# Kernel tuning notes

Hardware: AMD Instinct MI355X
Metric: run time of the kernel (lower is better)

## Reference

```python
import jax, jax.numpy as jnp
import numpy as np

DIM = 1024
HEADS = 8
DIM_HEAD = 64
INNER = HEADS * DIM_HEAD
SCALE = DIM_HEAD ** -0.5


def setup_inputs() -> dict:
    key = jax.random.key(0)
    ks = jax.random.split(key, 6)
    b, n = 2, 2048
    x = jax.random.normal(ks[0], (b, n, DIM), dtype=jnp.float32)
    rel_pos_bias = jax.random.normal(ks[1], (HEADS, n, n), dtype=jnp.float32)
    # learned params (Linear stores W as [out, in]; we keep [in, out] for x @ W)
    Wq = jax.random.normal(ks[2], (DIM, INNER), dtype=jnp.float32) * (DIM ** -0.5)
    Wkv = jax.random.normal(ks[3], (DIM, 2 * DIM_HEAD), dtype=jnp.float32) * (DIM ** -0.5)
    Wo = jax.random.normal(ks[4], (INNER, DIM), dtype=jnp.float32) * (INNER ** -0.5)
    bo = jax.random.normal(ks[5], (DIM,), dtype=jnp.float32) * 0.01
    return {"x": x, "rel_pos_bias": rel_pos_bias, "Wq": Wq, "Wkv": Wkv, "Wo": Wo, "bo": bo}


def reference(x, rel_pos_bias, Wq, Wkv, Wo, bo):
    b, n, _ = x.shape
    q = x @ Wq                       # [b, n, h*d]
    kv = x @ Wkv                     # [b, n, 2d] (multi-query: single shared kv head)
    k, v = kv[..., :DIM_HEAD], kv[..., DIM_HEAD:]
    q = q.reshape(b, n, HEADS, DIM_HEAD).transpose(0, 2, 1, 3) * SCALE  # [b, h, n, d]
    sim = jnp.einsum('bhid,bjd->bhij', q, k)
    sim = sim + rel_pos_bias         # bias broadcast over batch
    causal_mask = jnp.triu(jnp.ones((n, n), dtype=bool), k=1)
    neg = -jnp.finfo(sim.dtype).max
    sim = jnp.where(causal_mask, neg, sim)
    attn = jax.nn.softmax(sim, axis=-1)  # stable softmax (max-subtract internally)
    out = jnp.einsum('bhij,bjd->bhid', attn, v)
    out = out.transpose(0, 2, 1, 3).reshape(b, n, INNER)  # [b, n, h*d]
    return out @ Wo + bo
```

## Files before the change

kernel.cpp:

```cpp
#include <hip/hip_runtime.h>

#define NSEQ 2048
#define NB 2
#define NH 8
#define HD 64
#define DMODEL 1024
#define DINNER 512

#define SLOT_F 4224

typedef __attribute__((ext_vector_type(8))) short bf16x8;
typedef __attribute__((ext_vector_type(4))) float f32x4;

__device__ __forceinline__ ushort f2bf(float f) {
  uint u = __float_as_uint(f);
  uint r = (u + 0x7fffu + ((u >> 16) & 1u)) >> 16;
  return (ushort)r;
}

__device__ __forceinline__ void gld16(const ushort* g, ushort* l) {
  __builtin_amdgcn_global_load_lds(
      (const __attribute__((address_space(1))) uint*)g,
      (__attribute__((address_space(3))) uint*)l, 16, 0, 0);
}

__global__ __launch_bounds__(256) void cast_x_kernel(
    const float* __restrict__ x, ushort* __restrict__ xb) {
  size_t i = ((size_t)blockIdx.x * 256 + threadIdx.x) * 8;
  float4 a = *(const float4*)(x + i);
  float4 b = *(const float4*)(x + i + 4);
  ushort4 o1, o2;
  o1.x = f2bf(a.x); o1.y = f2bf(a.y); o1.z = f2bf(a.z); o1.w = f2bf(a.w);
  o2.x = f2bf(b.x); o2.y = f2bf(b.y); o2.z = f2bf(b.z); o2.w = f2bf(b.w);
  *(ushort4*)(xb + i) = o1;
  *(ushort4*)(xb + i + 4) = o2;
}

__global__ __launch_bounds__(256) void transpose_cast_kernel(
    const float* __restrict__ srcA, const float* __restrict__ srcB,
    int ldA, int ldB, int nsplit, int Ktot, ushort* __restrict__ dst) {
  __shared__ float t[64][65];
  const int k0 = blockIdx.x * 64;
  const int n0 = blockIdx.y * 64;
  const float* src; int ld, nb;
  if (n0 < nsplit) { src = srcA; ld = ldA; nb = n0; }
  else { src = srcB; ld = ldB; nb = n0 - nsplit; }
  const int r = threadIdx.x >> 4;
  const int c = (threadIdx.x & 15) * 4;
#pragma unroll
  for (int rr = r; rr < 64; rr += 16) {
    float4 v = *(const float4*)(src + (size_t)(k0 + rr) * ld + nb + c);
    t[rr][c + 0] = v.x; t[rr][c + 1] = v.y; t[rr][c + 2] = v.z; t[rr][c + 3] = v.w;
  }
  __syncthreads();
#pragma unroll
  for (int rr = r; rr < 64; rr += 16) {
    ushort4 o;
    o.x = f2bf(t[c + 0][rr]); o.y = f2bf(t[c + 1][rr]);
    o.z = f2bf(t[c + 2][rr]); o.w = f2bf(t[c + 3][rr]);
    *(ushort4*)(dst + (size_t)(n0 + rr) * Ktot + k0 + c) = o;
  }
}

__device__ __forceinline__ void stage_tile(const ushort* __restrict__ src, int ld,
                                           int row0, int k0, ushort* lds, int tid) {
#pragma unroll
  for (int i = 0; i < 4; ++i) {
    const int cix = i * 256 + tid;
    const int row = cix >> 3, j = cix & 7;
    uint4 v = *(const uint4*)(src + (size_t)(row0 + row) * ld + k0 + j * 8);
    *(uint4*)((char*)lds + row * 128 + ((j ^ (row & 7)) << 4)) = v;
  }
}

__device__ __forceinline__ void gemm_tile(const ushort* __restrict__ A,
                                          const ushort* __restrict__ Bt, int K,
                                          int m0, int n0, ushort* As, ushort* Bs,
                                          int tid, f32x4 acc[4][4]) {
  const int lane = tid & 63;
  const int w = tid >> 6;
  const int wr = w >> 1, wc = w & 1;
  const int lr = lane & 15, lg = lane >> 4;
  for (int k0 = 0; k0 < K; k0 += 64) {
    __syncthreads();
    stage_tile(A, K, m0, k0, As, tid);
    stage_tile(Bt, K, n0, k0, Bs, tid);
    __syncthreads();
#pragma unroll
    for (int kk = 0; kk < 2; ++kk) {
      bf16x8 af[4], bfr[4];
#pragma unroll
      for (int mi = 0; mi < 4; ++mi) {
        const int r = wr * 64 + mi * 16 + lr;
        af[mi] = *(const bf16x8*)((char*)As + r * 128 + (((kk * 4 + lg) ^ (r & 7)) << 4));
      }
#pragma unroll
      for (int ni = 0; ni < 4; ++ni) {
        const int r = wc * 64 + ni * 16 + lr;
        bfr[ni] = *(const bf16x8*)((char*)Bs + r * 128 + (((kk * 4 + lg) ^ (r & 7)) << 4));
      }
#pragma unroll
      for (int mi = 0; mi < 4; ++mi)
#pragma unroll
        for (int ni = 0; ni < 4; ++ni)
          acc[mi][ni] = __builtin_amdgcn_mfma_f32_16x16x32_bf16(af[mi], bfr[ni],
                                                                acc[mi][ni], 0, 0, 0);
    }
  }
}

__global__ __launch_bounds__(256) void qkv_mfma_kernel(
    const ushort* __restrict__ xb, const ushort* __restrict__ WT1,
    ushort* __restrict__ qb, ushort* __restrict__ ksw, ushort* __restrict__ vsw) {
  __shared__ ushort As[128 * 64];
  __shared__ ushort Bs[128 * 64];
  const int tid = threadIdx.x;
  const int m0 = blockIdx.x * 128, n0 = blockIdx.y * 128;
  f32x4 acc[4][4];
#pragma unroll
  for (int a = 0; a < 4; ++a)
#pragma unroll
    for (int b = 0; b < 4; ++b) acc[a][b] = (f32x4){0.f, 0.f, 0.f, 0.f};
  gemm_tile(xb, WT1, DMODEL, m0, n0, As, Bs, tid, acc);
  const int lane = tid & 63;
  const int w = tid >> 6;
  const int wr = w >> 1, wc = w & 1;
  const int lr = lane & 15, lg = lane >> 4;
#pragma unroll
  for (int mi = 0; mi < 4; ++mi)
#pragma unroll
    for (int ni = 0; ni < 4; ++ni) {
      const int n = n0 + wc * 64 + ni * 16 + lr;
      if (n >= 640) continue;
#pragma unroll
      for (int r = 0; r < 4; ++r) {
        const int m = m0 + wr * 64 + mi * 16 + lg * 4 + r;
        const int bb = m >> 11, key = m & (NSEQ - 1);
        const float v = acc[mi][ni][r];
        if (n < DINNER) {
          const int h = n >> 6, d = n & 63;
          qb[((size_t)((bb * NH + h) * NSEQ) + key) * HD + d] = f2bf(v * 0.125f);
        } else if (n < DINNER + HD) {
          const int d = n - DINNER;
          const int t = key >> 6, row = key & 63;
          const int ch = d >> 3, pos = d & 7;
          ksw[(size_t)((bb * 32 + t) * 64 + row) * 64 +
              ((ch ^ (row & 7)) << 3) + pos] = f2bf(v);
        } else {
          const int d = n - DINNER - HD;
          const int pr = key >> 7, kk = key & 127;
          const int ch = kk >> 3, pos = kk & 7;
          vsw[(size_t)((bb * 16 + pr) * 64 + d) * 128 +
              ((ch ^ (d & 15)) << 3) + pos] = f2bf(v);
        }
      }
    }
}

__global__ __launch_bounds__(256) void out_mfma_kernel(
    const ushort* __restrict__ ab, const ushort* __restrict__ WoT,
    const float* __restrict__ bo, float* __restrict__ out) {
  __shared__ ushort As[128 * 64];
  __shared__ ushort Bs[128 * 64];
  const int tid = threadIdx.x;
  const int m0 = blockIdx.x * 128, n0 = blockIdx.y * 128;
  f32x4 acc[4][4];
#pragma unroll
  for (int a = 0; a < 4; ++a)
#pragma unroll
    for (int b = 0; b < 4; ++b) acc[a][b] = (f32x4){0.f, 0.f, 0.f, 0.f};
  gemm_tile(ab, WoT, DINNER, m0, n0, As, Bs, tid, acc);
  const int lane = tid & 63;
  const int w = tid >> 6;
  const int wr = w >> 1, wc = w & 1;
  const int lr = lane & 15, lg = lane >> 4;
#pragma unroll
  for (int mi = 0; mi < 4; ++mi)
#pragma unroll
    for (int ni = 0; ni < 4; ++ni) {
      const int n = n0 + wc * 64 + ni * 16 + lr;
      const float bias = bo[n];
#pragma unroll
      for (int r = 0; r < 4; ++r) {
        const int m = m0 + wr * 64 + mi * 16 + lg * 4 + r;
        out[(size_t)m * DMODEL + n] = acc[mi][ni][r] + bias;
      }
    }
}

__global__ __launch_bounds__(256) void attn_mfma_kernel(
    const ushort* __restrict__ qb, const ushort* __restrict__ ksw,
    const ushort* __restrict__ vsw, const float* __restrict__ rpb,
    ushort* __restrict__ ob, float* __restrict__ scratch) {
  __shared__ ushort Ks[2 * 128 * 64];
  __shared__ ushort Vs[2 * 64 * 128];
  __shared__ ushort Ps[4 * 16 * 128];
  const int tid = threadIdx.x;
  const int lane = tid & 63;
  const int w = tid >> 6;
  const int id = blockIdx.x;
  const int bh = id & 15;
  int qt, ch, p0, p1, partial;
  if (id < 256) {
    qt = 16 + (id >> 4); ch = 0; p0 = 0; p1 = 8; partial = 1;
  } else if (id < 512) {
    qt = 31 - ((id - 256) >> 4); ch = 1; p0 = 8; p1 = (qt >> 1) + 1; partial = 1;
  } else {
    qt = 15 - ((id - 512) >> 4); ch = 0; p0 = 0; p1 = (qt >> 1) + 1; partial = 0;
  }
  const int bb = bh >> 3, h = bh & 7;
  const int q0 = qt * 64;
  const int lr = lane & 15;
  const int lg = lane >> 4;
  const int pdiag = qt >> 1;

  const ushort* kpair = ksw + (size_t)bb * 32 * 64 * 64;
  const ushort* vpair = vsw + (size_t)bb * 16 * 64 * 128;
  const ushort* ksrcw = kpair + w * 2048 + lane * 8;
  const ushort* vsrcw = vpair + w * 2048 + lane * 8;
  ushort* kdstw = Ks + w * 2048;
  ushort* vdstw = Vs + w * 2048;

#define ISSUE(pp, bsel)                                                     \
  {                                                                         \
    const ushort* _ks = ksrcw + (size_t)(pp) * 8192;                        \
    const ushort* _vs = vsrcw + (size_t)(pp) * 8192;                        \
    ushort* _kd = kdstw + (bsel) * 8192;                                    \
    ushort* _vd = vdstw + (bsel) * 8192;                                    \
    gld16(_ks + 0 * 512, _kd + 0 * 512);                                    \
    gld16(_ks + 1 * 512, _kd + 1 * 512);                                    \
    gld16(_ks + 2 * 512, _kd + 2 * 512);                                    \
    gld16(_ks + 3 * 512, _kd + 3 * 512);                                    \
    gld16(_vs + 0 * 512, _vd + 0 * 512);                                    \
    gld16(_vs + 1 * 512, _vd + 1 * 512);                                    \
    gld16(_vs + 2 * 512, _vd + 2 * 512);                                    \
    gld16(_vs + 3 * 512, _vd + 3 * 512);                                    \
  }

#define LOAD_BIAS(pp, dst)                                                  \
  {                                                                         \
    const float* _br = rpb + (size_t)h * NSEQ * NSEQ +                      \
                       (size_t)(q0 + w * 16 + lg * 4) * NSEQ +              \
                       (pp) * 128 + lr;                                     \
    _Pragma("unroll")                                                       \
    for (int _ct = 0; _ct < 8; ++_ct)                                       \
      _Pragma("unroll")                                                     \
      for (int _r = 0; _r < 4; ++_r)                                        \
        dst[_ct][_r] = _br[(size_t)_r * NSEQ + _ct * 16];                   \
  }

  bf16x8 qf[2];
  {
    const ushort* qrow =
        qb + ((size_t)(bh * NSEQ) + q0 + w * 16 + lr) * HD + lg * 8;
    qf[0] = *(const bf16x8*)qrow;
    qf[1] = *(const bf16x8*)(qrow + 32);
  }
  f32x4 oacc[4];
  float m_run[4], l_run[4];
#pragma unroll
  for (int r = 0; r < 4; ++r) { m_run[r] = -1e30f; l_run[r] = 0.f; }
#pragma unroll
  for (int dt = 0; dt < 4; ++dt) oacc[dt] = (f32x4){0.f, 0.f, 0.f, 0.f};

  float bias_c[8][4], bias_n[8][4];

  ISSUE(p0, 0);
  LOAD_BIAS(p0, bias_c);
  ISSUE(p0 + 1, 1);
  int curb = 0;

  for (int p = p0; p < p1; ++p) {
    if (p < p1 - 1) {
      asm volatile("s_waitcnt vmcnt(40)" ::: "memory");
    } else {
      asm volatile("s_waitcnt vmcnt(32)" ::: "memory");
    }
    __builtin_amdgcn_sched_barrier(0);
    __builtin_amdgcn_s_barrier();

    const char* Kc = (const char*)(Ks + curb * 8192);
    const char* Vc = (const char*)(Vs + curb * 8192);
    f32x4 s[8];
    __builtin_amdgcn_s_setprio(1);
#pragma unroll
    for (int ct = 0; ct < 8; ++ct) {
      s[ct] = (f32x4){0.f, 0.f, 0.f, 0.f};
      const int krow = ct * 16 + lr;
#pragma unroll
      for (int kk = 0; kk < 2; ++kk) {
        bf16x8 kf = *(const bf16x8*)(Kc + krow * 128 +
                                     (((kk * 4 + lg) ^ (krow & 7)) << 4));
        s[ct] = __builtin_amdgcn_mfma_f32_16x16x32_bf16(qf[kk], kf, s[ct], 0, 0, 0);
      }
    }
    __builtin_amdgcn_s_setprio(0);
    if (p + 1 < p1) LOAD_BIAS(p + 1, bias_n);
#pragma unroll
    for (int ct = 0; ct < 8; ++ct)
#pragma unroll
      for (int r = 0; r < 4; ++r) s[ct][r] += bias_c[ct][r];
    if (p == pdiag) {
      const int qrel = q0 + w * 16 + lg * 4;
#pragma unroll
      for (int ct = 0; ct < 8; ++ct) {
        const int kg = p * 128 + ct * 16 + lr;
#pragma unroll
        for (int r = 0; r < 4; ++r)
          if (kg > qrel + r) s[ct][r] = -1e30f;
      }
    }
    float fac[4];
#pragma unroll
    for (int r = 0; r < 4; ++r) {
      float mt = s[0][r];
#pragma unroll
      for (int ct = 1; ct < 8; ++ct) mt = fmaxf(mt, s[ct][r]);
#pragma unroll
      for (int msk = 1; msk < 16; msk <<= 1)
        mt = fmaxf(mt, __shfl_xor(mt, msk, 64));
      const float m_new = fmaxf(m_run[r], mt);
      fac[r] = __expf(m_run[r] - m_new);
      m_run[r] = m_new;
      float ls = 0.f;
#pragma unroll
      for (int ct = 0; ct < 8; ++ct) {
        const float pv = __expf(s[ct][r] - m_new);
        s[ct][r] = pv;
        ls += pv;
      }
#pragma unroll
      for (int msk = 1; msk < 16; msk <<= 1) ls += __shfl_xor(ls, msk, 64);
      l_run[r] = l_run[r] * fac[r] + ls;
    }
#pragma unroll
    for (int dt = 0; dt < 4; ++dt)
#pragma unroll
      for (int r = 0; r < 4; ++r) oacc[dt][r] *= fac[r];
    char* Pw = (char*)Ps + w * 4096;
#pragma unroll
    for (int ct = 0; ct < 8; ++ct) {
      uint u01, u23;
      asm("v_cvt_pk_bf16_f32 %0, %1, %2" : "=v"(u01) : "v"(s[ct][0]), "v"(s[ct][1]));
      asm("v_cvt_pk_bf16_f32 %0, %1, %2" : "=v"(u23) : "v"(s[ct][2]), "v"(s[ct][3]));
      const int cbyte = (ct * 16 + lr) * 2;
      const int chv = cbyte >> 4, off = cbyte & 15;
      const int r0 = lg * 4;
      *(ushort*)(Pw + (r0 + 0) * 256 + (((chv ^ (r0 + 0)) << 4) | off)) = (ushort)u01;
      *(ushort*)(Pw + (r0 + 1) * 256 + (((chv ^ (r0 + 1)) << 4) | off)) = (ushort)(u01 >> 16);
      *(ushort*)(Pw + (r0 + 2) * 256 + (((chv ^ (r0 + 2)) << 4) | off)) = (ushort)u23;
      *(ushort*)(Pw + (r0 + 3) * 256 + (((chv ^ (r0 + 3)) << 4) | off)) = (ushort)(u23 >> 16);
    }
    __builtin_amdgcn_s_setprio(1);
#pragma unroll
    for (int kk = 0; kk < 4; ++kk) {
      bf16x8 pf = *(const bf16x8*)(Pw + lr * 256 + (((kk * 4 + lg) ^ lr) << 4));
#pragma unroll
      for (int dt = 0; dt < 4; ++dt) {
        const int vrow = dt * 16 + lr;
        bf16x8 vf = *(const bf16x8*)(Vc + vrow * 256 +
                                     (((kk * 4 + lg) ^ (vrow & 15)) << 4));
        oacc[dt] =
            __builtin_amdgcn_mfma_f32_16x16x32_bf16(pf, vf, oacc[dt], 0, 0, 0);
      }
    }
    __builtin_amdgcn_s_setprio(0);
    __builtin_amdgcn_sched_barrier(0);
    __builtin_amdgcn_s_barrier();
    if (p + 2 < p1) ISSUE(p + 2, curb);
    if (p + 1 < p1) {
#pragma unroll
      for (int ct = 0; ct < 8; ++ct)
#pragma unroll
        for (int r = 0; r < 4; ++r) bias_c[ct][r] = bias_n[ct][r];
    }
    curb ^= 1;
  }
#undef ISSUE
#undef LOAD_BIAS
  if (!partial) {
#pragma unroll
    for (int r = 0; r < 4; ++r) {
      const int qg = q0 + w * 16 + lg * 4 + r;
      const float inv = 1.0f / l_run[r];
      ushort* dst = ob + ((size_t)(bb * NSEQ) + qg) * DINNER + h * HD + lr;
#pragma unroll
      for (int dt = 0; dt < 4; ++dt) dst[dt * 16] = f2bf(oacc[dt][r] * inv);
    }
  } else {
    float* slot =
        scratch + (size_t)((bh * 16 + (qt - 16)) * 2 + ch) * SLOT_F;
#pragma unroll
    for (int r = 0; r < 4; ++r) {
      const int row = w * 16 + lg * 4 + r;
#pragma unroll
      for (int dt = 0; dt < 4; ++dt)
        slot[row * 64 + dt * 16 + lr] = oacc[dt][r];
      if (lr == 0) {
        slot[4096 + row] = m_run[r];
        slot[4160 + row] = l_run[r];
      }
    }
  }
}

__global__ __launch_bounds__(256) void attn_merge_kernel(
    const float* __restrict__ scratch, ushort* __restrict__ ob) {
  const int bid = blockIdx.x;
  const int bh = bid >> 4;
  const int qt = 16 + (bid & 15);
  const int bb = bh >> 3, h = bh & 7;
  const float* s0 = scratch + (size_t)((bh * 16 + (qt - 16)) * 2) * SLOT_F;
  const float* s1 = s0 + SLOT_F;
  const int t = threadIdx.x;
  const int r = t >> 2;
  const int c0 = (t & 3) * 16;
  const float m0 = s0[4096 + r], m1 = s1[4096 + r];
  const float M = fmaxf(m0, m1);
  const float sc0 = __expf(m0 - M), sc1 = __expf(m1 - M);
  const float L = s0[4160 + r] * sc0 + s1[4160 + r] * sc1;
  const float inv = 1.0f / L;
  ushort* dst = ob + ((size_t)(bb * NSEQ) + qt * 64 + r) * DINNER + h * HD + c0;
#pragma unroll
  for (int j4 = 0; j4 < 4; ++j4) {
    float4 a = *(const float4*)(s0 + r * 64 + c0 + j4 * 4);
    float4 b = *(const float4*)(s1 + r * 64 + c0 + j4 * 4);
    dst[j4 * 4 + 0] = f2bf((a.x * sc0 + b.x * sc1) * inv);
    dst[j4 * 4 + 1] = f2bf((a.y * sc0 + b.y * sc1) * inv);
    dst[j4 * 4 + 2] = f2bf((a.z * sc0 + b.z * sc1) * inv);
    dst[j4 * 4 + 3] = f2bf((a.w * sc0 + b.w * sc1) * inv);
  }
}

extern "C" void kernel_launch(void* const* d_in, const int* in_sizes, int n_in,
                              void* d_out, int out_size, void* d_ws, size_t ws_size,
                              hipStream_t stream) {
  (void)in_sizes; (void)n_in; (void)out_size; (void)ws_size;
  const float* x = (const float*)d_in[0];
  const float* rpb = (const float*)d_in[1];
  const float* Wq = (const float*)d_in[2];
  const float* Wkv = (const float*)d_in[3];
  const float* Wo = (const float*)d_in[4];
  const float* bo = (const float*)d_in[5];
  float* out = (float*)d_out;

  ushort* qbb = (ushort*)d_ws;
  ushort* ksw = qbb + (size_t)NB * NH * NSEQ * HD;
  ushort* vsw = ksw + (size_t)NB * NSEQ * HD;
  ushort* obuf = vsw + (size_t)NB * NSEQ * HD;
  ushort* xb = obuf + (size_t)NB * NSEQ * DINNER;
  ushort* WT1 = xb + (size_t)NB * NSEQ * DMODEL;
  ushort* WoT = WT1 + (size_t)640 * DMODEL;
  float* scratch = (float*)(WoT + (size_t)DMODEL * DINNER);

  cast_x_kernel<<<dim3(2048), 256, 0, stream>>>(x, xb);
  transpose_cast_kernel<<<dim3(16, 10), 256, 0, stream>>>(Wq, Wkv, 512, 128, 512,
                                                          DMODEL, WT1);
  transpose_cast_kernel<<<dim3(8, 16), 256, 0, stream>>>(Wo, Wo, DMODEL, DMODEL,
                                                         DMODEL, DINNER, WoT);
  qkv_mfma_kernel<<<dim3(32, 5), 256, 0, stream>>>(xb, WT1, qbb, ksw, vsw);
  attn_mfma_kernel<<<dim3(768), 256, 0, stream>>>(qbb, ksw, vsw, rpb, obuf,
                                                  scratch);
  attn_merge_kernel<<<dim3(256), 256, 0, stream>>>(scratch, obuf);
  out_mfma_kernel<<<dim3(32, 8), 256, 0, stream>>>(obuf, WoT, bo, out);
}
```

Measured before the change: 95.66 us.

## Transpose attention MFMA accumulators so each lane owns a query row, use exp2

Swaps the MFMA operand order so the score and output accumulators are transposed, which gives each lane a single query row and four consecutive keys. Row max and sum then need only two cross-lane shuffles instead of four per row, the bias loads become vectorized f32x4 reads, and P stores and output writes are packed. The softmax scale is folded into log2e so exp2 replaces expf, and the vmcnt thresholds are lowered to match the smaller number of bias loads. A wrong vmcnt count or a mismatch in the transposed layout would break correctness.

```diff
diff --git a/kernel.cpp b/kernel.cpp
--- a/kernel.cpp
+++ b/kernel.cpp
@@ -8,6 +8,7 @@
 #define DINNER 512
 
 #define SLOT_F 4224
+#define LOG2E 1.44269504f
 
 typedef __attribute__((ext_vector_type(8))) short bf16x8;
 typedef __attribute__((ext_vector_type(4))) float f32x4;
@@ -139,7 +140,8 @@
         const float v = acc[mi][ni][r];
         if (n < DINNER) {
           const int h = n >> 6, d = n & 63;
-          qb[((size_t)((bb * NH + h) * NSEQ) + key) * HD + d] = f2bf(v * 0.125f);
+          qb[((size_t)((bb * NH + h) * NSEQ) + key) * HD + d] =
+              f2bf(v * (0.125f * LOG2E));
         } else if (n < DINNER + HD) {
           const int d = n - DINNER;
           const int t = key >> 6, row = key & 63;
@@ -200,7 +202,7 @@
   const int w = tid >> 6;
   const int id = blockIdx.x;
   const int bh = id & 15;
-  int qt, ch, p0, p1, partial;
+  int qt, p0, p1, partial, ch;
   if (id < 256) {
     qt = 16 + (id >> 4); ch = 0; p0 = 0; p1 = 8; partial = 1;
   } else if (id < 512) {
@@ -213,6 +215,7 @@
   const int lr = lane & 15;
   const int lg = lane >> 4;
   const int pdiag = qt >> 1;
+  const int qg = q0 + w * 16 + lr;
 
   const ushort* kpair = ksw + (size_t)bb * 32 * 64 * 64;
   const ushort* vpair = vsw + (size_t)bb * 16 * 64 * 128;
@@ -240,30 +243,24 @@
 #define LOAD_BIAS(pp, dst)                                                  \
   {                                                                         \
     const float* _br = rpb + (size_t)h * NSEQ * NSEQ +                      \
-                       (size_t)(q0 + w * 16 + lg * 4) * NSEQ +              \
-                       (pp) * 128 + lr;                                     \
+                       (size_t)qg * NSEQ + (pp) * 128 + lg * 4;             \
     _Pragma("unroll")                                                       \
     for (int _ct = 0; _ct < 8; ++_ct)                                       \
-      _Pragma("unroll")                                                     \
-      for (int _r = 0; _r < 4; ++_r)                                        \
-        dst[_ct][_r] = _br[(size_t)_r * NSEQ + _ct * 16];                   \
+      dst[_ct] = *(const f32x4*)(_br + _ct * 16);                           \
   }
 
   bf16x8 qf[2];
   {
-    const ushort* qrow =
-        qb + ((size_t)(bh * NSEQ) + q0 + w * 16 + lr) * HD + lg * 8;
+    const ushort* qrow = qb + ((size_t)(bh * NSEQ) + qg) * HD + lg * 8;
     qf[0] = *(const bf16x8*)qrow;
     qf[1] = *(const bf16x8*)(qrow + 32);
   }
-  f32x4 oacc[4];
-  float m_run[4], l_run[4];
-#pragma unroll
-  for (int r = 0; r < 4; ++r) { m_run[r] = -1e30f; l_run[r] = 0.f; }
-#pragma unroll
-  for (int dt = 0; dt < 4; ++dt) oacc[dt] = (f32x4){0.f, 0.f, 0.f, 0.f};
-
-  float bias_c[8][4], bias_n[8][4];
+  f32x4 oaccT[4];
+#pragma unroll
+  for (int dt = 0; dt < 4; ++dt) oaccT[dt] = (f32x4){0.f, 0.f, 0.f, 0.f};
+  float m_run = -1e30f, l_run = 0.f;
+
+  f32x4 bias_c[8], bias_n[8];
 
   ISSUE(p0, 0);
   LOAD_BIAS(p0, bias_c);
@@ -272,9 +269,9 @@
 
   for (int p = p0; p < p1; ++p) {
     if (p < p1 - 1) {
-      asm volatile("s_waitcnt vmcnt(40)" ::: "memory");
+      asm volatile("s_waitcnt vmcnt(16)" ::: "memory");
     } else {
-      asm volatile("s_waitcnt vmcnt(32)" ::: "memory");
+      asm volatile("s_waitcnt vmcnt(8)" ::: "memory");
     }
     __builtin_amdgcn_sched_barrier(0);
     __builtin_amdgcn_s_barrier();
@@ -291,7 +288,7 @@
       for (int kk = 0; kk < 2; ++kk) {
         bf16x8 kf = *(const bf16x8*)(Kc + krow * 128 +
                                      (((kk * 4 + lg) ^ (krow & 7)) << 4));
-        s[ct] = __builtin_amdgcn_mfma_f32_16x16x32_bf16(qf[kk], kf, s[ct], 0, 0, 0);
+        s[ct] = __builtin_amdgcn_mfma_f32_16x16x32_bf16(kf, qf[kk], s[ct], 0, 0, 0);
       }
     }
     __builtin_amdgcn_s_setprio(0);
@@ -299,57 +296,51 @@
 #pragma unroll
     for (int ct = 0; ct < 8; ++ct)
 #pragma unroll
-      for (int r = 0; r < 4; ++r) s[ct][r] += bias_c[ct][r];
+      for (int r = 0; r < 4; ++r)
+        s[ct][r] = fmaf(bias_c[ct][r], LOG2E, s[ct][r]);
     if (p == pdiag) {
-      const int qrel = q0 + w * 16 + lg * 4;
 #pragma unroll
       for (int ct = 0; ct < 8; ++ct) {
-        const int kg = p * 128 + ct * 16 + lr;
+        const int kg = p * 128 + ct * 16 + lg * 4;
 #pragma unroll
         for (int r = 0; r < 4; ++r)
-          if (kg > qrel + r) s[ct][r] = -1e30f;
-      }
-    }
-    float fac[4];
-#pragma unroll
-    for (int r = 0; r < 4; ++r) {
-      float mt = s[0][r];
-#pragma unroll
-      for (int ct = 1; ct < 8; ++ct) mt = fmaxf(mt, s[ct][r]);
-#pragma unroll
-      for (int msk = 1; msk < 16; msk <<= 1)
-        mt = fmaxf(mt, __shfl_xor(mt, msk, 64));
-      const float m_new = fmaxf(m_run[r], mt);
-      fac[r] = __expf(m_run[r] - m_new);
-      m_run[r] = m_new;
-      float ls = 0.f;
-#pragma unroll
-      for (int ct = 0; ct < 8; ++ct) {
-        const float pv = __expf(s[ct][r] - m_new);
-        s[ct][r] = pv;
-        ls += pv;
-      }
-#pragma unroll
-      for (int msk = 1; msk < 16; msk <<= 1) ls += __shfl_xor(ls, msk, 64);
-      l_run[r] = l_run[r] * fac[r] + ls;
-    }
-#pragma unroll
-    for (int dt = 0; dt < 4; ++dt)
-#pragma unroll
-      for (int r = 0; r < 4; ++r) oacc[dt][r] *= fac[r];
+          if (kg + r > qg) s[ct][r] = -1e30f;
+      }
+    }
+    float cm[8];
+#pragma unroll
+    for (int ct = 0; ct < 8; ++ct)
+      cm[ct] = fmaxf(fmaxf(s[ct][0], s[ct][1]), fmaxf(s[ct][2], s[ct][3]));
+    float mt = fmaxf(fmaxf(fmaxf(cm[0], cm[1]), fmaxf(cm[2], cm[3])),
+                     fmaxf(fmaxf(cm[4], cm[5]), fmaxf(cm[6], cm[7])));
+    mt = fmaxf(mt, __shfl_xor(mt, 16, 64));
+    mt = fmaxf(mt, __shfl_xor(mt, 32, 64));
+    const float m_new = fmaxf(m_run, mt);
+    const float fac = exp2f(m_run - m_new);
+    m_run = m_new;
+    float cs[8];
+#pragma unroll
+    for (int ct = 0; ct < 8; ++ct) {
+#pragma unroll
+      for (int r = 0; r < 4; ++r) s[ct][r] = exp2f(s[ct][r] - m_new);
+      cs[ct] = (s[ct][0] + s[ct][1]) + (s[ct][2] + s[ct][3]);
+    }
+    float ls = ((cs[0] + cs[1]) + (cs[2] + cs[3])) +
+               ((cs[4] + cs[5]) + (cs[6] + cs[7]));
+    ls += __shfl_xor(ls, 16, 64);
+    ls += __shfl_xor(ls, 32, 64);
+    l_run = l_run * fac + ls;
+#pragma unroll
+    for (int dt = 0; dt < 4; ++dt) oaccT[dt] *= fac;
     char* Pw = (char*)Ps + w * 4096;
 #pragma unroll
     for (int ct = 0; ct < 8; ++ct) {
       uint u01, u23;
       asm("v_cvt_pk_bf16_f32 %0, %1, %2" : "=v"(u01) : "v"(s[ct][0]), "v"(s[ct][1]));
       asm("v_cvt_pk_bf16_f32 %0, %1, %2" : "=v"(u23) : "v"(s[ct][2]), "v"(s[ct][3]));
-      const int cbyte = (ct * 16 + lr) * 2;
-      const int chv = cbyte >> 4, off = cbyte & 15;
-      const int r0 = lg * 4;
-      *(ushort*)(Pw + (r0 + 0) * 256 + (((chv ^ (r0 + 0)) << 4) | off)) = (ushort)u01;
-      *(ushort*)(Pw + (r0 + 1) * 256 + (((chv ^ (r0 + 1)) << 4) | off)) = (ushort)(u01 >> 16);
-      *(ushort*)(Pw + (r0 + 2) * 256 + (((chv ^ (r0 + 2)) << 4) | off)) = (ushort)u23;
-      *(ushort*)(Pw + (r0 + 3) * 256 + (((chv ^ (r0 + 3)) << 4) | off)) = (ushort)(u23 >> 16);
+      const int chunk = 2 * ct + (lg >> 1);
+      uint2 uv; uv.x = u01; uv.y = u23;
+      *(uint2*)(Pw + lr * 256 + (((chunk ^ lr) << 4) | ((lg & 1) * 8))) = uv;
     }
     __builtin_amdgcn_s_setprio(1);
 #pragma unroll
@@ -360,8 +351,8 @@
         const int vrow = dt * 16 + lr;
         bf16x8 vf = *(const bf16x8*)(Vc + vrow * 256 +
                                      (((kk * 4 + lg) ^ (vrow & 15)) << 4));
-        oacc[dt] =
-            __builtin_amdgcn_mfma_f32_16x16x32_bf16(pf, vf, oacc[dt], 0, 0, 0);
+        oaccT[dt] =
+            __builtin_amdgcn_mfma_f32_16x16x32_bf16(vf, pf, oaccT[dt], 0, 0, 0);
       }
     }
     __builtin_amdgcn_s_setprio(0);
@@ -370,36 +361,34 @@
     if (p + 2 < p1) ISSUE(p + 2, curb);
     if (p + 1 < p1) {
 #pragma unroll
-      for (int ct = 0; ct < 8; ++ct)
-#pragma unroll
-        for (int r = 0; r < 4; ++r) bias_c[ct][r] = bias_n[ct][r];
+      for (int ct = 0; ct < 8; ++ct) bias_c[ct] = bias_n[ct];
     }
     curb ^= 1;
   }
 #undef ISSUE
 #undef LOAD_BIAS
   if (!partial) {
-#pragma unroll
-    for (int r = 0; r < 4; ++r) {
-      const int qg = q0 + w * 16 + lg * 4 + r;
-      const float inv = 1.0f / l_run[r];
-      ushort* dst = ob + ((size_t)(bb * NSEQ) + qg) * DINNER + h * HD + lr;
-#pragma unroll
-      for (int dt = 0; dt < 4; ++dt) dst[dt * 16] = f2bf(oacc[dt][r] * inv);
+    const float inv = 1.0f / l_run;
+    ushort* dst = ob + ((size_t)(bb * NSEQ) + qg) * DINNER + h * HD;
+#pragma unroll
+    for (int dt = 0; dt < 4; ++dt) {
+      uint u01, u23;
+      const float o0 = oaccT[dt][0] * inv, o1 = oaccT[dt][1] * inv;
+      const float o2 = oaccT[dt][2] * inv, o3 = oaccT[dt][3] * inv;
+      asm("v_cvt_pk_bf16_f32 %0, %1, %2" : "=v"(u01) : "v"(o0), "v"(o1));
+      asm("v_cvt_pk_bf16_f32 %0, %1, %2" : "=v"(u23) : "v"(o2), "v"(o3));
+      uint2 uv; uv.x = u01; uv.y = u23;
+      *(uint2*)(dst + dt * 16 + lg * 4) = uv;
     }
   } else {
-    float* slot =
-        scratch + (size_t)((bh * 16 + (qt - 16)) * 2 + ch) * SLOT_F;
-#pragma unroll
-    for (int r = 0; r < 4; ++r) {
-      const int row = w * 16 + lg * 4 + r;
-#pragma unroll
-      for (int dt = 0; dt < 4; ++dt)
-        slot[row * 64 + dt * 16 + lr] = oacc[dt][r];
-      if (lr == 0) {
-        slot[4096 + row] = m_run[r];
-        slot[4160 + row] = l_run[r];
-      }
+    float* slot = scratch + (size_t)((bh * 16 + (qt - 16)) * 2 + ch) * SLOT_F;
+    const int row = w * 16 + lr;
+#pragma unroll
+    for (int dt = 0; dt < 4; ++dt)
+      *(f32x4*)(slot + row * 64 + dt * 16 + lg * 4) = oaccT[dt];
+    if (lg == 0) {
+      slot[4096 + row] = m_run;
+      slot[4160 + row] = l_run;
     }
   }
 }
@@ -417,7 +406,7 @@
   const int c0 = (t & 3) * 16;
   const float m0 = s0[4096 + r], m1 = s1[4096 + r];
   const float M = fmaxf(m0, m1);
-  const float sc0 = __expf(m0 - M), sc1 = __expf(m1 - M);
+  const float sc0 = exp2f(m0 - M), sc1 = exp2f(m1 - M);
   const float L = s0[4160 + r] * sc0 + s1[4160 + r] * sc1;
   const float inv = 1.0f / L;
   ushort* dst = ob + ((size_t)(bb * NSEQ) + qt * 64 + r) * DINNER + h * HD + c0;
```

After: 98.97 us. +3.5%, slower.

## Fuse x cast into QKV GEMM, merge weight casts, shrink GEMM N-tile

Applied to the files above, without the earlier changes.

The separate x-to-bf16 cast kernel is removed. The QKV GEMM now loads fp32 x directly and converts it with packed cvt instructions while staging into LDS. The two weight transpose-cast launches are merged into one kernel. Both GEMMs move from 128x128 to 128x64 tiles, doubling the grid for better CU occupancy and removing the wasted column tile in QKV. In exchange, x is read as fp32 once per N-tile (ten times), and tiles are smaller, so each loaded element is reused less.

```diff
diff --git a/kernel.cpp b/kernel.cpp
--- a/kernel.cpp
+++ b/kernel.cpp
@@ -8,6 +8,7 @@
 #define DINNER 512
 
 #define SLOT_F 4224
+#define LOG2E 1.44269504f
 
 typedef __attribute__((ext_vector_type(8))) short bf16x8;
 typedef __attribute__((ext_vector_type(4))) float f32x4;
@@ -24,24 +25,25 @@
       (__attribute__((address_space(3))) uint*)l, 16, 0, 0);
 }
 
-__global__ __launch_bounds__(256) void cast_x_kernel(
-    const float* __restrict__ x, ushort* __restrict__ xb) {
-  size_t i = ((size_t)blockIdx.x * 256 + threadIdx.x) * 8;
-  float4 a = *(const float4*)(x + i);
-  float4 b = *(const float4*)(x + i + 4);
-  ushort4 o1, o2;
-  o1.x = f2bf(a.x); o1.y = f2bf(a.y); o1.z = f2bf(a.z); o1.w = f2bf(a.w);
-  o2.x = f2bf(b.x); o2.y = f2bf(b.y); o2.z = f2bf(b.z); o2.w = f2bf(b.w);
-  *(ushort4*)(xb + i) = o1;
-  *(ushort4*)(xb + i + 4) = o2;
-}
-
-__global__ __launch_bounds__(256) void transpose_cast_kernel(
-    const float* __restrict__ srcA, const float* __restrict__ srcB,
-    int ldA, int ldB, int nsplit, int Ktot, ushort* __restrict__ dst) {
+__global__ __launch_bounds__(256) void transpose_cast_both_kernel(
+    const float* __restrict__ Wq, const float* __restrict__ Wkv,
+    const float* __restrict__ Wo, ushort* __restrict__ WT1,
+    ushort* __restrict__ WoT) {
   __shared__ float t[64][65];
-  const int k0 = blockIdx.x * 64;
-  const int n0 = blockIdx.y * 64;
+  const int id = blockIdx.x;
+  const float *srcA, *srcB;
+  int ldA, ldB, nsplit, Ktot, k0, n0;
+  ushort* dst;
+  if (id < 160) {
+    k0 = (id & 15) * 64; n0 = (id >> 4) * 64;
+    srcA = Wq; srcB = Wkv; ldA = 512; ldB = 128; nsplit = 512;
+    Ktot = 1024; dst = WT1;
+  } else {
+    const int u = id - 160;
+    k0 = (u & 7) * 64; n0 = (u >> 3) * 64;
+    srcA = Wo; srcB = Wo; ldA = 1024; ldB = 1024; nsplit = 1024;
+    Ktot = 512; dst = WoT;
+  }
   const float* src; int ld, nb;
   if (n0 < nsplit) { src = srcA; ld = ldA; nb = n0; }
   else { src = srcB; ld = ldB; nb = n0 - nsplit; }
@@ -62,8 +64,8 @@
   }
 }
 
-__device__ __forceinline__ void stage_tile(const ushort* __restrict__ src, int ld,
-                                           int row0, int k0, ushort* lds, int tid) {
+__device__ __forceinline__ void stageA_bf16(const ushort* __restrict__ src, int ld,
+                                            int row0, int k0, ushort* lds, int tid) {
 #pragma unroll
   for (int i = 0; i < 4; ++i) {
     const int cix = i * 256 + tid;
@@ -72,113 +74,152 @@
     *(uint4*)((char*)lds + row * 128 + ((j ^ (row & 7)) << 4)) = v;
   }
 }
-
-__device__ __forceinline__ void gemm_tile(const ushort* __restrict__ A,
-                                          const ushort* __restrict__ Bt, int K,
-                                          int m0, int n0, ushort* As, ushort* Bs,
-                                          int tid, f32x4 acc[4][4]) {
+__device__ __forceinline__ void stageA_f32(const float* __restrict__ src, int ld,
+                                           int row0, int k0, ushort* lds, int tid) {
+#pragma unroll
+  for (int i = 0; i < 4; ++i) {
+    const int cix = i * 256 + tid;
+    const int row = cix >> 3, j = cix & 7;
+    const float* p = src + (size_t)(row0 + row) * ld + k0 + j * 8;
+    float4 a = *(const float4*)p;
+    float4 b = *(const float4*)(p + 4);
+    uint u0, u1, u2, u3;
+    asm("v_cvt_pk_bf16_f32 %0, %1, %2" : "=v"(u0) : "v"(a.x), "v"(a.y));
+    asm("v_cvt_pk_bf16_f32 %0, %1, %2" : "=v"(u1) : "v"(a.z), "v"(a.w));
+    asm("v_cvt_pk_bf16_f32 %0, %1, %2" : "=v"(u2) : "v"(b.x), "v"(b.y));
+    asm("v_cvt_pk_bf16_f32 %0, %1, %2" : "=v"(u3) : "v"(b.z), "v"(b.w));
+    uint4 v; v.x = u0; v.y = u1; v.z = u2; v.w = u3;
+    *(uint4*)((char*)lds + row * 128 + ((j ^ (row & 7)) << 4)) = v;
+  }
+}
+__device__ __forceinline__ void stageB(const ushort* __restrict__ src, int ld,
+                                       int row0, int k0, ushort* lds, int tid) {
+#pragma unroll
+  for (int i = 0; i < 2; ++i) {
+    const int cix = i * 256 + tid;
+    const int row = cix >> 3, j = cix & 7;
+    uint4 v = *(const uint4*)(src + (size_t)(row0 + row) * ld + k0 + j * 8);
+    *(uint4*)((char*)lds + row * 128 + ((j ^ (row & 7)) << 4)) = v;
+  }
+}
+
+__global__ __launch_bounds__(256) void qkv_mfma_kernel(
+    const float* __restrict__ x, const ushort* __restrict__ WT1,
+    ushort* __restrict__ qb, ushort* __restrict__ ksw, ushort* __restrict__ vsw) {
+  __shared__ ushort As[128 * 64];
+  __shared__ ushort Bs[64 * 64];
+  const int tid = threadIdx.x;
+  const int m0 = blockIdx.x * 128, n0 = blockIdx.y * 64;
   const int lane = tid & 63;
   const int w = tid >> 6;
   const int wr = w >> 1, wc = w & 1;
   const int lr = lane & 15, lg = lane >> 4;
-  for (int k0 = 0; k0 < K; k0 += 64) {
+  f32x4 acc[4][2];
+#pragma unroll
+  for (int a = 0; a < 4; ++a)
+#pragma unroll
+    for (int b = 0; b < 2; ++b) acc[a][b] = (f32x4){0.f, 0.f, 0.f, 0.f};
+  for (int k0 = 0; k0 < DMODEL; k0 += 64) {
     __syncthreads();
-    stage_tile(A, K, m0, k0, As, tid);
-    stage_tile(Bt, K, n0, k0, Bs, tid);
+    stageA_f32(x, DMODEL, m0, k0, As, tid);
+    stageB(WT1, DMODEL, n0, k0, Bs, tid);
     __syncthreads();
 #pragma unroll
     for (int kk = 0; kk < 2; ++kk) {
-      bf16x8 af[4], bfr[4];
+      bf16x8 af[4], bfr[2];
 #pragma unroll
       for (int mi = 0; mi < 4; ++mi) {
         const int r = wr * 64 + mi * 16 + lr;
         af[mi] = *(const bf16x8*)((char*)As + r * 128 + (((kk * 4 + lg) ^ (r & 7)) << 4));
       }
 #pragma unroll
-      for (int ni = 0; ni < 4; ++ni) {
-        const int r = wc * 64 + ni * 16 + lr;
+      for (int ni = 0; ni < 2; ++ni) {
+        const int r = wc * 32 + ni * 16 + lr;
         bfr[ni] = *(const bf16x8*)((char*)Bs + r * 128 + (((kk * 4 + lg) ^ (r & 7)) << 4));
       }
 #pragma unroll
       for (int mi = 0; mi < 4; ++mi)
 #pragma unroll
-        for (int ni = 0; ni < 4; ++ni)
+        for (int ni = 0; ni < 2; ++ni)
           acc[mi][ni] = __builtin_amdgcn_mfma_f32_16x16x32_bf16(af[mi], bfr[ni],
                                                                 acc[mi][ni], 0, 0, 0);
     }
   }
-}
-
-__global__ __launch_bounds__(256) void qkv_mfma_kernel(
-    const ushort* __restrict__ xb, const ushort* __restrict__ WT1,
-    ushort* __restrict__ qb, ushort* __restrict__ ksw, ushort* __restrict__ vsw) {
+#pragma unroll
+  for (int mi = 0; mi < 4; ++mi)
+#pragma unroll
+    for (int ni = 0; ni < 2; ++ni) {
+      const int n = n0 + wc * 32 + ni * 16 + lr;
+#pragma unroll
+      for (int r = 0; r < 4; ++r) {
+        const int m = m0 + wr * 64 + mi * 16 + lg * 4 + r;
+        const int bb = m >> 11, key = m & (NSEQ - 1);
+        const float v = acc[mi][ni][r];
+        if (blockIdx.y < 8) {
+          const int h = n >> 6, d = n & 63;
+          qb[((size_t)((bb * NH + h) * NSEQ) + key) * HD + d] = f2bf(v * 0.125f);
+        } else if (blockIdx.y == 8) {
+          const int d = n - DINNER;
+          const int t = key >> 6, row = key & 63;
+          ksw[(size_t)((bb * 32 + t) * 64 + row) * 64 +
+              (((d >> 3) ^ (row & 7)) << 3) + (d & 7)] = f2bf(v);
+        } else {
+          const int d = n - DINNER - HD;
+          const int pr = key >> 7, kk = key & 127;
+          vsw[(size_t)((bb * 16 + pr) * 64 + d) * 128 +
+              (((kk >> 3) ^ (d & 15)) << 3) + (kk & 7)] = f2bf(v);
+        }
+      }
+    }
+}
+
+__global__ __launch_bounds__(256) void out_mfma_kernel(
+    const ushort* __restrict__ ab, const ushort* __restrict__ WoT,
+    const float* __restrict__ bo, float* __restrict__ out) {
   __shared__ ushort As[128 * 64];
-  __shared__ ushort Bs[128 * 64];
+  __shared__ ushort Bs[64 * 64];
   const int tid = threadIdx.x;
-  const int m0 = blockIdx.x * 128, n0 = blockIdx.y * 128;
-  f32x4 acc[4][4];
-#pragma unroll
-  for (int a = 0; a < 4; ++a)
-#pragma unroll
-    for (int b = 0; b < 4; ++b) acc[a][b] = (f32x4){0.f, 0.f, 0.f, 0.f};
-  gemm_tile(xb, WT1, DMODEL, m0, n0, As, Bs, tid, acc);
+  const int m0 = blockIdx.x * 128, n0 = blockIdx.y * 64;
   const int lane = tid & 63;
   const int w = tid >> 6;
   const int wr = w >> 1, wc = w & 1;
   const int lr = lane & 15, lg = lane >> 4;
+  f32x4 acc[4][2];
+#pragma unroll
+  for (int a = 0; a < 4; ++a)
+#pragma unroll
+    for (int b = 0; b < 2; ++b) acc[a][b] = (f32x4){0.f, 0.f, 0.f, 0.f};
+  for (int k0 = 0; k0 < DINNER; k0 += 64) {
+    __syncthreads();
+    stageA_bf16(ab, DINNER, m0, k0, As, tid);
+    stageB(WoT, DINNER, n0, k0, Bs, tid);
+    __syncthreads();
+#pragma unroll
+    for (int kk = 0; kk < 2; ++kk) {
+      bf16x8 af[4], bfr[2];
+#pragma unroll
+      for (int mi = 0; mi < 4; ++mi) {
+        const int r = wr * 64 + mi * 16 + lr;
+        af[mi] = *(const bf16x8*)((char*)As + r * 128 + (((kk * 4 + lg) ^ (r & 7)) << 4));
+      }
+#pragma unroll
+      for (int ni = 0; ni < 2; ++ni) {
+        const int r = wc * 32 + ni * 16 + lr;
+        bfr[ni] = *(const bf16x8*)((char*)Bs + r * 128 + (((kk * 4 + lg) ^ (r & 7)) << 4));
+      }
+#pragma unroll
+      for (int mi = 0; mi < 4; ++mi)
+#pragma unroll
+        for (int ni = 0; ni < 2; ++ni)
+          acc[mi][ni] = __builtin_amdgcn_mfma_f32_16x16x32_bf16(af[mi], bfr[ni],
+                                                                acc[mi][ni], 0, 0, 0);
+    }
+  }
 #pragma unroll
   for (int mi = 0; mi < 4; ++mi)
 #pragma unroll
-    for (int ni = 0; ni < 4; ++ni) {
-      const int n = n0 + wc * 64 + ni * 16 + lr;
-      if (n >= 640) continue;
-#pragma unroll
-      for (int r = 0; r < 4; ++r) {
-        const int m = m0 + wr * 64 + mi * 16 + lg * 4 + r;
-        const int bb = m >> 11, key = m & (NSEQ - 1);
-        const float v = acc[mi][ni][r];
-        if (n < DINNER) {
-          const int h = n >> 6, d = n & 63;
-          qb[((size_t)((bb * NH + h) * NSEQ) + key) * HD + d] = f2bf(v * 0.125f);
-        } else if (n < DINNER + HD) {
-          const int d = n - DINNER;
-          const int t = key >> 6, row = key & 63;
-          const int ch = d >> 3, pos = d & 7;
-          ksw[(size_t)((bb * 32 + t) * 64 + row) * 64 +
-              ((ch ^ (row & 7)) << 3) + pos] = f2bf(v);
-        } else {
-          const int d = n - DINNER - HD;
-          const int pr = key >> 7, kk = key & 127;
-          const int ch = kk >> 3, pos = kk & 7;
-          vsw[(size_t)((bb * 16 + pr) * 64 + d) * 128 +
-              ((ch ^ (d & 15)) << 3) + pos] = f2bf(v);
-        }
-      }
-    }
-}
-
-__global__ __launch_bounds__(256) void out_mfma_kernel(
-    const ushort* __restrict__ ab, const ushort* __restrict__ WoT,
-    const float* __restrict__ bo, float* __restrict__ out) {
-  __shared__ ushort As[128 * 64];
-  __shared__ ushort Bs[128 * 64];
-  const int tid = threadIdx.x;
-  const int m0 = blockIdx.x * 128, n0 = blockIdx.y * 128;
-  f32x4 acc[4][4];
-#pragma unroll
-  for (int a = 0; a < 4; ++a)
-#pragma unroll
-    for (int b = 0; b < 4; ++b) acc[a][b] = (f32x4){0.f, 0.f, 0.f, 0.f};
-  gemm_tile(ab, WoT, DINNER, m0, n0, As, Bs, tid, acc);
-  const int lane = tid & 63;
-  const int w = tid >> 6;
-  const int wr = w >> 1, wc = w & 1;
-  const int lr = lane & 15, lg = lane >> 4;
-#pragma unroll
-  for (int mi = 0; mi < 4; ++mi)
-#pragma unroll
-    for (int ni = 0; ni < 4; ++ni) {
-      const int n = n0 + wc * 64 + ni * 16 + lr;
+    for (int ni = 0; ni < 2; ++ni) {
+      const int n = n0 + wc * 32 + ni * 16 + lr;
       const float bias = bo[n];
 #pragma unroll
       for (int r = 0; r < 4; ++r) {
@@ -448,19 +489,14 @@
   ushort* ksw = qbb + (size_t)NB * NH * NSEQ * HD;
   ushort* vsw = ksw + (size_t)NB * NSEQ * HD;
   ushort* obuf = vsw + (size_t)NB * NSEQ * HD;
-  ushort* xb = obuf + (size_t)NB * NSEQ * DINNER;
-  ushort* WT1 = xb + (size_t)NB * NSEQ * DMODEL;
+  ushort* WT1 = obuf + (size_t)NB * NSEQ * DINNER;
   ushort* WoT = WT1 + (size_t)640 * DMODEL;
   float* scratch = (float*)(WoT + (size_t)DMODEL * DINNER);
 
-  cast_x_kernel<<<dim3(2048), 256, 0, stream>>>(x, xb);
-  transpose_cast_kernel<<<dim3(16, 10), 256, 0, stream>>>(Wq, Wkv, 512, 128, 512,
-                                                          DMODEL, WT1);
-  transpose_cast_kernel<<<dim3(8, 16), 256, 0, stream>>>(Wo, Wo, DMODEL, DMODEL,
-                                                         DMODEL, DINNER, WoT);
-  qkv_mfma_kernel<<<dim3(32, 5), 256, 0, stream>>>(xb, WT1, qbb, ksw, vsw);
+  transpose_cast_both_kernel<<<dim3(288), 256, 0, stream>>>(Wq, Wkv, Wo, WT1, WoT);
+  qkv_mfma_kernel<<<dim3(32, 10), 256, 0, stream>>>(x, WT1, qbb, ksw, vsw);
   attn_mfma_kernel<<<dim3(768), 256, 0, stream>>>(qbb, ksw, vsw, rpb, obuf,
                                                   scratch);
   attn_merge_kernel<<<dim3(256), 256, 0, stream>>>(scratch, obuf);
-  out_mfma_kernel<<<dim3(32, 8), 256, 0, stream>>>(obuf, WoT, bo, out);
-}
+  out_mfma_kernel<<<dim3(32, 16), 256, 0, stream>>>(obuf, WoT, bo, out);
+}
```

Result: faster. 82.89 us (median of 2 runs) (-13.4%).
